# Kernel tuning notes

Measured on AMD Instinct MI355X. Metric: run time of the kernel, lower is better.

Reference implementation:

```python
import jax, jax.numpy as jnp
import numpy as np

B, C, V, K, H, W = 1, 3, 9, 8, 512, 512


def setup_inputs() -> dict:
    key = jax.random.key(0)
    k0, k1 = jax.random.split(key, 2)
    x = jax.random.normal(k0, (B, C, K, H, W), jnp.float32)          # FDL layers (spatial)
    y_views = jax.random.normal(k1, (B, C, V, H, W), jnp.float32)    # observed views (spatial)
    g = jnp.arange(3, dtype=jnp.float32) - 1.0                       # 3x3 camera grid positions
    uu, vv = jnp.meshgrid(g, g, indexing='ij')
    u = uu.reshape(-1)
    v = vv.reshape(-1)
    d = jnp.linspace(-2.0, 2.0, K).astype(jnp.float32)               # d_fdl disparities
    rho = jnp.full((1,), 0.3, jnp.float32)
    return {"x": x, "y_views": y_views, "u": u, "v": v, "d": d, "rho": rho}


def _pack_half_spectrum(Xf, x_c, y_c, n_proc):
    # [..., H, W] -> transpose to [..., W, H], center-roll so zero freq is at (x_c-1, y_c-1),
    # flatten x-major, keep the non-redundant half spectrum (first n_proc entries).
    Xt = jnp.swapaxes(Xf, -1, -2)
    Xt = jnp.roll(Xt, shift=(x_c - 1, y_c - 1), axis=(-2, -1))
    sh = Xt.shape
    return Xt.reshape(sh[:-2] + (sh[-2] * sh[-1],))[..., :n_proc]


def reference(x, y_views, u, v, d, rho):
    Bn, Cn, Kn = x.shape[0], x.shape[1], x.shape[2]
    Hn, Wn = x.shape[-2], x.shape[-1]
    rho = rho.reshape(())
    x_c = (Wn + 2) // 2                      # ceil((W+1)/2)
    y_c = (Hn + 2) // 2
    n_proc = Hn * (x_c - 1) + y_c            # half-spectrum size
    e0 = 1 - Hn % 2
    e1 = 1 - Wn % 2

    X = jnp.fft.fft2(x)                      # [B,C,K,H,W] complex64
    Y = jnp.fft.fft2(y_views)                # [B,C,V,H,W] complex64
    Xp = jnp.moveaxis(_pack_half_spectrum(X, x_c, y_c, n_proc), 2, 3) * rho   # [B,C,F,K]
    Yp = jnp.moveaxis(_pack_half_spectrum(Y, x_c, y_c, n_proc), 2, 3)         # [B,C,F,V]

    # centered angular frequency grids, flattened x-major to match packing order
    wx = (jnp.arange(Wn, dtype=jnp.float32) - (x_c - 1)) * (2.0 * np.pi / Wn)
    wy = (jnp.arange(Hn, dtype=jnp.float32) - (y_c - 1)) * (2.0 * np.pi / Hn)
    wx_f = jnp.repeat(wx, Hn)[:n_proc]       # [F]
    wy_f = jnp.tile(wy, Wn)[:n_proc]         # [F]

    # FDL data matrix A[f,v,k] = exp(i * d_k * (u_v*wx_f + v_v*wy_f))
    shift = u[None, :] * wx_f[:, None] + v[None, :] * wy_f[:, None]   # [F,V]
    A = jnp.exp(1j * shift[:, :, None] * d[None, None, :])            # [F,V,K] complex64
    Ah = jnp.conj(A)
    ATA = jnp.einsum('fvk,fvl->fkl', Ah, A)                           # [F,K,K]
    ATb = jnp.einsum('fvk,bcfv->bcfk', Ah, Yp)                        # [B,C,F,K]
    M = ATA + rho * jnp.eye(Kn, dtype=ATA.dtype)
    fdl = jnp.linalg.solve(M, (ATb + Xp)[..., None])[..., 0]          # [B,C,F,K]

    # pad redundant half with zeros, restore [B,C,K,H,W] layout
    fdl = jnp.pad(fdl, ((0, 0), (0, 0), (0, Hn * Wn - n_proc), (0, 0)))
    fdl = fdl.reshape(Bn, Cn, Wn, Hn, Kn).transpose(0, 1, 4, 3, 2)    # [B,C,K,H,W]

    # Hermitian (conjugate) symmetry reconstruction
    fdl = fdl.at[..., y_c:, x_c - 1:].set(jnp.conj(fdl[..., e0:y_c - 1, e1:x_c][..., ::-1, ::-1]))
    fdl = fdl.at[..., e0:y_c, x_c:].set(jnp.conj(fdl[..., y_c - 1:, e1:x_c - 1][..., ::-1, ::-1]))
    fdl = jnp.roll(fdl, shift=(1 - y_c, 1 - x_c), axis=(-2, -1))
    return jnp.fft.ifft2(fdl).real
```

## Files before the change

kernel.cpp:

```cpp
#include <hip/hip_runtime.h>
#include <math.h>

constexpr int N    = 512;
constexpr int LOGN = 9;
constexpr int NN   = N * N;
constexpr int CCH  = 3;
constexpr int KK   = 8;
constexpr int VV   = 9;
constexpr int FHALF = N * (N / 2) + (N / 2 + 1);
constexpr float PI_F = 3.14159265358979323846f;

__device__ __forceinline__ float2 cmulf(float2 a, float2 b) {
    return make_float2(a.x * b.x - a.y * b.y, a.x * b.y + a.y * b.x);
}
__device__ __forceinline__ float2 cadd(float2 a, float2 b) { return make_float2(a.x + b.x, a.y + b.y); }
__device__ __forceinline__ float2 csub(float2 a, float2 b) { return make_float2(a.x - b.x, a.y - b.y); }

template<int SG>
__device__ __forceinline__ float2 cmuli(float2 z) {
    return (SG < 0) ? make_float2(z.y, -z.x) : make_float2(-z.y, z.x);
}

template<int SG>
__device__ __forceinline__ void dft8(float2 x[8]) {
    const float c = 0.70710678118654752440f;
    float2 a0 = cadd(x[0], x[4]), a1 = cadd(x[1], x[5]);
    float2 a2 = cadd(x[2], x[6]), a3 = cadd(x[3], x[7]);
    float2 d0 = csub(x[0], x[4]), d1 = csub(x[1], x[5]);
    float2 d2 = csub(x[2], x[6]), d3 = csub(x[3], x[7]);
    float2 b0 = d0;
    float2 b1 = cmulf(d1, make_float2(c, (float)SG * c));
    float2 b2 = cmuli<SG>(d2);
    float2 b3 = cmulf(d3, make_float2(-c, (float)SG * c));
    float2 aa0 = cadd(a0, a2), aa1 = cadd(a1, a3);
    float2 ab0 = csub(a0, a2), ab1 = cmuli<SG>(csub(a1, a3));
    float2 ba0 = cadd(b0, b2), ba1 = cadd(b1, b3);
    float2 bb0 = csub(b0, b2), bb1 = cmuli<SG>(csub(b1, b3));
    x[0] = cadd(aa0, aa1); x[4] = csub(aa0, aa1);
    x[2] = cadd(ab0, ab1); x[6] = csub(ab0, ab1);
    x[1] = cadd(ba0, ba1); x[5] = csub(ba0, ba1);
    x[3] = cadd(bb0, bb1); x[7] = csub(bb0, bb1);
}

__device__ __forceinline__ void twiddle8(float2 v[8], float base) {
    float sn, cs;
    __sincosf(base, &sn, &cs);
    float2 w1 = make_float2(cs, sn);
    float2 wk = w1;
    v[1] = cmulf(v[1], wk);
    #pragma unroll
    for (int k = 2; k < 8; ++k) { wk = cmulf(wk, w1); v[k] = cmulf(v[k], wk); }
}

template<int SG>
__device__ __forceinline__ void wave_fft512(float2 v[8], float* sre, float* sim,
                                            int t, int stride, int off) {
    int t1 = t >> 3, t0 = t & 7;
    dft8<SG>(v);
    twiddle8(v, (float)SG * (2.0f * PI_F / 512.0f) * (float)t);
    #pragma unroll
    for (int k = 0; k < 8; ++k) {
        int a = (68 * k + 8 * t1 + t0) * stride + off;
        sre[a] = v[k].x; sim[a] = v[k].y;
    }
    #pragma unroll
    for (int n = 0; n < 8; ++n) {
        int a = (68 * t1 + 8 * n + t0) * stride + off;
        v[n] = make_float2(sre[a], sim[a]);
    }
    dft8<SG>(v);
    twiddle8(v, (float)SG * (2.0f * PI_F / 64.0f) * (float)t0);
    #pragma unroll
    for (int k = 0; k < 8; ++k) {
        int a = (68 * t0 + 8 * k + t1) * stride + off;
        sre[a] = v[k].x; sim[a] = v[k].y;
    }
    #pragma unroll
    for (int n = 0; n < 8; ++n) {
        int a = (68 * n + 8 * t0 + t1) * stride + off;
        v[n] = make_float2(sre[a], sim[a]);
    }
    dft8<SG>(v);
}

__global__ __launch_bounds__(256) void k_fft_r2c_rows_pack(const float* __restrict__ inx,
                                                           const float* __restrict__ iny,
                                                           int nximg,
                                                           float2* __restrict__ out) {
    __shared__ float sre[4][544];
    __shared__ float sim[4][544];
    int w = threadIdx.x >> 6, t = threadIdx.x & 63;
    long long gp = (long long)blockIdx.x * 4 + w;
    long long row0 = gp * 2;
    long long xrows = (long long)nximg * N;
    const float* src0 = (row0 < xrows) ? (inx + row0 * N)
                                       : (iny + (row0 - xrows) * N);
    const float* src1 = src0 + N;
    float2 v[8];
    #pragma unroll
    for (int e = 0; e < 8; ++e) v[e] = make_float2(src0[t + 64 * e], src1[t + 64 * e]);
    wave_fft512<-1>(v, sre[w], sim[w], t, 1, 0);
    int kb = (t >> 3) + 8 * (t & 7);
    #pragma unroll
    for (int k0 = 0; k0 < 8; ++k0) {
        int p = kb + 64 * k0;
        sre[w][p] = v[k0].x; sim[w][p] = v[k0].y;
    }
    float2* dst0 = out + row0 * N;
    float2* dst1 = dst0 + N;
    #pragma unroll
    for (int k0 = 4; k0 < 8; ++k0) {
        int p  = kb + 64 * k0;
        int mp = 512 - p;
        float zmx = sre[w][mp], zmy = sim[w][mp];
        float2 Zp = v[k0];
        dst0[p] = make_float2(0.5f * (Zp.x + zmx), 0.5f * (Zp.y - zmy));
        dst1[p] = make_float2(0.5f * (Zp.y + zmy), 0.5f * (zmx - Zp.x));
    }
    if (t == 0) {
        dst0[0] = make_float2(v[0].x, 0.0f);
        dst1[0] = make_float2(v[0].y, 0.0f);
    }
}

__global__ __launch_bounds__(256) void k_fft_r2c_rows(const float* __restrict__ in,
                                                      float2* __restrict__ out) {
    __shared__ float sre[4][544];
    __shared__ float sim[4][544];
    int w = threadIdx.x >> 6, t = threadIdx.x & 63;
    long long grow = (long long)blockIdx.x * 4 + w;
    const float* src = in + grow * N;
    float2 v[8];
    #pragma unroll
    for (int e = 0; e < 8; ++e) v[e] = make_float2(src[t + 64 * e], 0.0f);
    wave_fft512<-1>(v, sre[w], sim[w], t, 1, 0);
    float2* dst = out + grow * N;
    int kb = (t >> 3) + 8 * (t & 7);
    #pragma unroll
    for (int k0 = 0; k0 < 8; ++k0) dst[kb + 64 * k0] = v[k0];
}

template<int SG>
__global__ __launch_bounds__(256) void k_fft_pairswap(float2* __restrict__ data,
                                                      float scale, int lex, int sex) {
    __shared__ float sre[4][544];
    __shared__ float sim[4][544];
    int w = threadIdx.x >> 6, t = threadIdx.x & 63;
    int b = blockIdx.x;
    long long imgBase = (long long)(b >> 7) * NN;
    int pa = (b & 127) << 1;
    int rowg = pa + (w & 1) + ((w >> 1) << 8);
    const float2* src = data + imgBase + (long long)rowg * N;
    float2 v[8];
    #pragma unroll
    for (int e = 0; e < 8; ++e) v[e] = src[t + 64 * (e ^ lex)];
    __syncthreads();
    wave_fft512<SG>(v, sre[w], sim[w], t, 1, 0);
    float2* dst = data + imgBase + (long long)(rowg ^ 256) * N;
    int kb = (t >> 3) + 8 * (t & 7);
    #pragma unroll
    for (int k0 = 0; k0 < 8; ++k0) {
        float2 z = v[k0];
        dst[kb + 64 * (k0 ^ sex)] = make_float2(z.x * scale, z.y * scale);
    }
}

__global__ __launch_bounds__(256) void k_fft_cols_fwd(const float2* __restrict__ in,
                                                      float2* __restrict__ out) {
    __shared__ float tre[4896];
    __shared__ float tim[4896];
    int t = threadIdx.x;
    long long imgOff = (long long)blockIdx.y * NN;
    int bx = blockIdx.x;
    int x0 = bx ? (248 + (bx << 3)) : 0;
    {
        int xi2 = (t & 3) << 1;
        int yb  = t >> 2;
        const float2* img = in + imgOff;
        #pragma unroll
        for (int it = 0; it < 8; ++it) {
            int y = it * 64 + yb;
            float4 q = *(const float4*)&img[(long long)y * N + x0 + xi2];
            int a = y * 9 + xi2;
            tre[a] = q.x; tim[a] = q.y; tre[a + 1] = q.z; tim[a + 1] = q.w;
        }
    }
    __syncthreads();
    int w = t >> 6, lane = t & 63;
    int kb = (lane >> 3) + 8 * (lane & 7);
    #pragma unroll
    for (int r = 0; r < 2; ++r) {
        int cc = (w << 1) | r;
        float2 v[8];
        #pragma unroll
        for (int e = 0; e < 8; ++e) {
            int a = (lane + 64 * e) * 9 + cc;
            v[e] = make_float2(tre[a], tim[a]);
        }
        wave_fft512<-1>(v, tre, tim, lane, 9, cc);
        #pragma unroll
        for (int k0 = 0; k0 < 8; ++k0) {
            int a = (kb + 64 * k0) * 9 + cc;
            tre[a] = v[k0].x; tim[a] = v[k0].y;
        }
    }
    __syncthreads();
    {
        int xi = t >> 5, co = t & 31;
        float2* orow = out + imgOff + (long long)((x0 + xi) ^ 256) * N;
        #pragma unroll
        for (int it = 0; it < 8; ++it) {
            int b = it * 64 + co * 2;
            int y1 = b ^ 256;
            int a1 = y1 * 9 + xi, a2 = (y1 + 1) * 9 + xi;
            *(float4*)&orow[b] = make_float4(tre[a1], tim[a1], tre[a2], tim[a2]);
        }
    }
}

__device__ __forceinline__ void accum_pair(float2 bacc[KK], float tr[KK], float s,
                                           float d0, float dlt, float2 Yp, float2 Yn) {
    float2 Sp = make_float2(Yp.x + Yn.x, Yp.y + Yn.y);
    float2 Dm = make_float2(Yp.x - Yn.x, Yp.y - Yn.y);
    float sn, cs;
    __sincosf(s * d0, &sn, &cs);  float2 p = make_float2(cs, sn);
    __sincosf(s * dlt, &sn, &cs); float2 q = make_float2(cs, sn);
    float2 w = q;
    #pragma unroll
    for (int k = 0; k < KK; ++k) {
        bacc[k].x += p.x * Sp.x + p.y * Dm.y;
        bacc[k].y += p.x * Sp.y - p.y * Dm.x;
        if (k < KK - 1) {
            p = cmulf(p, q);
            tr[k + 1] += 2.0f * w.x;
            w = cmulf(w, q);
        }
    }
}

__device__ __forceinline__ void solve_point(float2 bacc[KK], float tr[KK], float rho) {
    float diag = tr[0] + rho;
    float L[36], Li[KK];
    #pragma unroll
    for (int j = 0; j < KK; ++j) {
        float acc = diag;
        #pragma unroll
        for (int t = 0; t < j; ++t) { float l = L[(j * (j - 1)) / 2 + t]; acc -= l * l; }
        float dj = sqrtf(acc);
        float inv = 1.0f / dj;
        Li[j] = inv;
        #pragma unroll
        for (int i = j + 1; i < KK; ++i) {
            float a = tr[i - j];
            #pragma unroll
            for (int t = 0; t < j; ++t)
                a -= L[(i * (i - 1)) / 2 + t] * L[(j * (j - 1)) / 2 + t];
            L[(i * (i - 1)) / 2 + j] = a * inv;
        }
    }
    #pragma unroll
    for (int i = 0; i < KK; ++i) {
        float2 a = bacc[i];
        #pragma unroll
        for (int t = 0; t < i; ++t) {
            float l = L[(i * (i - 1)) / 2 + t];
            a.x -= l * bacc[t].x;
            a.y -= l * bacc[t].y;
        }
        bacc[i] = make_float2(a.x * Li[i], a.y * Li[i]);
    }
    #pragma unroll
    for (int i = KK - 1; i >= 0; --i) {
        float2 a = bacc[i];
        #pragma unroll
        for (int t = i + 1; t < KK; ++t) {
            float l = L[(t * (t - 1)) / 2 + i];
            a.x -= l * bacc[t].x;
            a.y -= l * bacc[t].y;
        }
        bacc[i] = make_float2(a.x * Li[i], a.y * Li[i]);
    }
}

__global__ __launch_bounds__(256) void k_solve_ifft(const float2* __restrict__ Xs,
                                                    const float2* __restrict__ Ys,
                                                    float2* __restrict__ P,
                                                    const float* __restrict__ uu,
                                                    const float* __restrict__ vv,
                                                    const float* __restrict__ dd,
                                                    const float* __restrict__ rhop) {
    __shared__ float gre[KK][N];
    __shared__ float gim[KK][N];
    __shared__ float fsre[4][544];
    __shared__ float fsim[4][544];
    int a  = blockIdx.x;
    int ch = blockIdx.y;
    int t  = threadIdx.x;
    float rho = rhop[0];
    float d0 = dd[0], dlt = dd[1] - dd[0];
    const float C = 2.0f * PI_F / (float)N;
    float wxv = (float)(a - 256) * C;
    const float2* Xrow = Xs + (long long)ch * KK * NN + (long long)a * N;
    const float2* Yrow = Ys + (long long)ch * VV * NN + (long long)a * N;
    float wy0 = (float)(t - 256) * C;
    float wy1 = (float)(t)       * C;

    float2 bacc0[KK], bacc1[KK];
    float tr0[KK], tr1[KK];
    {
        const float2* Yc = Yrow + (long long)4 * NN;
        float2 yc0 = Yc[t], yc1 = Yc[t + 256];
        #pragma unroll
        for (int k = 0; k < KK; ++k) { bacc0[k] = yc0; bacc1[k] = yc1; }
        tr0[0] = tr1[0] = (float)VV;
        #pragma unroll
        for (int l = 1; l < KK; ++l) { tr0[l] = 1.0f; tr1[l] = 1.0f; }
    }
    #pragma unroll
    for (int j = 0; j < 4; ++j) {
        int vp = 5 + j, vn = 3 - j;
        float su = uu[vp], sv = vv[vp];
        const float2* Ypr = Yrow + (long long)vp * NN;
        const float2* Ynr = Yrow + (long long)vn * NN;
        float2 Yp0 = Ypr[t], Yn0 = Ynr[t];
        float2 Yp1 = Ypr[t + 256], Yn1 = Ynr[t + 256];
        accum_pair(bacc0, tr0, su * wxv + sv * wy0, d0, dlt, Yp0, Yn0);
        accum_pair(bacc1, tr1, su * wxv + sv * wy1, d0, dlt, Yp1, Yn1);
    }
    #pragma unroll
    for (int k = 0; k < KK; ++k) {
        const float2* Xr = Xrow + (long long)k * NN;
        float2 x0v = Xr[t], x1v = Xr[t + 256];
        bacc0[k].x += rho * x0v.x; bacc0[k].y += rho * x0v.y;
        bacc1[k].x += rho * x1v.x; bacc1[k].y += rho * x1v.y;
    }
    solve_point(bacc0, tr0, rho);
    solve_point(bacc1, tr1, rho);
    #pragma unroll
    for (int k = 0; k < KK; ++k) {
        gre[k][t] = bacc0[k].x;       gim[k][t] = bacc0[k].y;
        gre[k][t + 256] = bacc1[k].x; gim[k][t + 256] = bacc1[k].y;
    }
    __syncthreads();
    if (a == 256 && t >= 1) {
        int b = t + 256, bs = 256 - t;
        #pragma unroll
        for (int k = 0; k < KK; ++k) {
            gre[k][b] = gre[k][bs];
            gim[k][b] = -gim[k][bs];
        }
    }
    __syncthreads();

    int w = t >> 6, lane = t & 63;
    int kb = (lane >> 3) + 8 * (lane & 7);
    float sgn = ((lane >> 3) & 1) ? -1.0f : 1.0f;
    const float inv512 = 1.0f / 512.0f;
    #pragma unroll
    for (int r = 0; r < 2; ++r) {
        int k = (w << 1) | r;
        float2 v[8];
        #pragma unroll
        for (int e = 0; e < 8; ++e) {
            int idx = (lane + 64 * e) ^ 256;
            v[e] = make_float2(gre[k][idx], gim[k][idx]);
        }
        wave_fft512<1>(v, fsre[w], fsim[w], lane, 1, 0);
        float s0x = gre[k][0], s0y = gim[k][0];
        float2* Pimg = P + (long long)(ch * KK + k) * NN;
        if (a >= 1 && a <= 255) {
            float2* pmain = Pimg + (long long)(a + 256) * N;
            float2* pmirr = Pimg + (long long)(256 - a) * N;
            #pragma unroll
            for (int k0 = 0; k0 < 8; ++k0) {
                int pos = kb + 64 * k0;
                float2 W = v[k0];
                pmain[pos] = make_float2(W.x * inv512, W.y * inv512);
                pmirr[pos] = make_float2((W.x - s0x * sgn) * inv512,
                                         (-W.y + s0y * sgn) * inv512);
            }
        } else {
            float2* pmain = Pimg + (long long)(a == 0 ? 256 : 0) * N;
            #pragma unroll
            for (int k0 = 0; k0 < 8; ++k0) {
                int pos = kb + 64 * k0;
                float2 W = v[k0];
                pmain[pos] = make_float2(W.x * inv512, W.y * inv512);
            }
        }
    }
}

__global__ __launch_bounds__(256) void k_fft_cols_inv_real(const float2* __restrict__ in,
                                                           float* __restrict__ out,
                                                           float scale) {
    __shared__ float tre[4896];
    __shared__ float tim[4896];
    int t = threadIdx.x;
    long long imgOff = (long long)blockIdx.y * NN;
    int b0 = blockIdx.x << 3;
    {
        int xi2 = (t & 3) << 1;
        int yb  = t >> 2;
        const float2* img = in + imgOff;
        #pragma unroll
        for (int it = 0; it < 8; ++it) {
            int c = it * 64 + yb;
            float4 q = *(const float4*)&img[(long long)c * N + b0 + xi2];
            int a = c * 9 + xi2;
            tre[a] = q.x; tim[a] = q.y; tre[a + 1] = q.z; tim[a + 1] = q.w;
        }
    }
    __syncthreads();
    int w = t >> 6, lane = t & 63;
    int kb = (lane >> 3) + 8 * (lane & 7);
    #pragma unroll
    for (int r = 0; r < 2; ++r) {
        int cc = (w << 1) | r;
        float2 v[8];
        #pragma unroll
        for (int e = 0; e < 8; ++e) {
            int a = (lane + 64 * e) * 9 + cc;
            v[e] = make_float2(tre[a], tim[a]);
        }
        wave_fft512<1>(v, tre, tim, lane, 9, cc);
        #pragma unroll
        for (int k0 = 0; k0 < 8; ++k0)
            tre[(kb + 64 * k0) * 9 + cc] = v[k0].x;
    }
    __syncthreads();
    {
        int xi = t >> 5, co = t & 31;
        float* orow = out + (long long)blockIdx.y * NN + (long long)(b0 + xi) * N;
        #pragma unroll
        for (int it = 0; it < 4; ++it) {
            int ww = it * 128 + co * 4;
            *(float4*)&orow[ww] = make_float4(tre[ww * 9 + xi] * scale,
                                              tre[(ww + 1) * 9 + xi] * scale,
                                              tre[(ww + 2) * 9 + xi] * scale,
                                              tre[(ww + 3) * 9 + xi] * scale);
        }
    }
}

__global__ __launch_bounds__(256) void k_transpose_inplace(float2* __restrict__ data) {
    int ti = blockIdx.x, tj = blockIdx.y;
    if (ti > tj) return;
    float2* img = data + (long long)blockIdx.z * NN;
    __shared__ float2 ta[32][33];
    __shared__ float2 tb[32][33];
    int tx = threadIdx.x, ty = threadIdx.y;
    int r0 = ti << 5, c0 = tj << 5;
    bool diag = (ti == tj);
    #pragma unroll
    for (int kk = 0; kk < 4; ++kk) {
        int r = ty + (kk << 3);
        ta[r][tx] = img[(long long)(r0 + r) * N + (c0 + tx)];
        if (!diag) tb[r][tx] = img[(long long)(c0 + r) * N + (r0 + tx)];
    }
    __syncthreads();
    #pragma unroll
    for (int kk = 0; kk < 4; ++kk) {
        int r = ty + (kk << 3);
        img[(long long)(c0 + r) * N + (r0 + tx)] = ta[tx][r];
        if (!diag) img[(long long)(r0 + r) * N + (c0 + tx)] = tb[tx][r];
    }
}

__global__ __launch_bounds__(256) void k_fft_c2r_rows(const float2* __restrict__ in,
                                                      float* __restrict__ out, float scale) {
    __shared__ float sre[4][544];
    __shared__ float sim[4][544];
    int w = threadIdx.x >> 6, t = threadIdx.x & 63;
    long long grow = (long long)blockIdx.x * 4 + w;
    const float2* src = in + grow * N;
    float2 v[8];
    #pragma unroll
    for (int e = 0; e < 8; ++e) v[e] = src[t + 64 * e];
    wave_fft512<1>(v, sre[w], sim[w], t, 1, 0);
    float* dst = out + grow * N;
    int kb = (t >> 3) + 8 * (t & 7);
    #pragma unroll
    for (int k0 = 0; k0 < 8; ++k0) dst[kb + 64 * k0] = v[k0].x * scale;
}

__global__ __launch_bounds__(256) void k_solve(float2* __restrict__ Xs,
                                               const float2* __restrict__ Ys,
                                               const float* __restrict__ uu,
                                               const float* __restrict__ vv,
                                               const float* __restrict__ dd,
                                               const float* __restrict__ rhop) {
    int f = blockIdx.x * 256 + threadIdx.x;
    if (f >= FHALF) return;
    long long coffX = (long long)blockIdx.y * KK * NN;
    long long coffY = (long long)blockIdx.y * VV * NN;
    float rho = rhop[0];
    int x = f >> LOGN;
    int y = f & (N - 1);
    float wxv = (float)(x - N / 2) * (2.0f * PI_F / (float)N);
    float wyv = (float)(y - N / 2) * (2.0f * PI_F / (float)N);
    float d0 = dd[0], dlt = dd[1] - dd[0];
    float2 bacc[KK];
    float tr[KK];
    {
        float2 Yc = Ys[coffY + (long long)4 * NN + f];
        #pragma unroll
        for (int k = 0; k < KK; ++k) bacc[k] = Yc;
        tr[0] = (float)VV;
        #pragma unroll
        for (int l = 1; l < KK; ++l) tr[l] = 1.0f;
    }
    #pragma unroll
    for (int j = 0; j < 4; ++j) {
        int vp = 5 + j, vn = 3 - j;
        float s = uu[vp] * wxv + vv[vp] * wyv;
        accum_pair(bacc, tr, s, d0, dlt,
                   Ys[coffY + (long long)vp * NN + f],
                   Ys[coffY + (long long)vn * NN + f]);
    }
    #pragma unroll
    for (int k = 0; k < KK; ++k) {
        float2 Xk = Xs[coffX + (long long)k * NN + f];
        bacc[k].x += rho * Xk.x;
        bacc[k].y += rho * Xk.y;
    }
    solve_point(bacc, tr, rho);
    int xm = (N - x) & (N - 1);
    int ym = (N - y) & (N - 1);
    long long fm = (long long)xm * N + ym;
    bool conjMirror = false, zeroMirror = false;
    if (x >= 1 && x <= N / 2 - 1) {
        if (y == 0) zeroMirror = true; else conjMirror = true;
    } else if (x == N / 2 && y >= 1 && y <= N / 2 - 1) {
        conjMirror = true;
    }
    #pragma unroll
    for (int k = 0; k < KK; ++k) {
        float2* base = Xs + coffX + (long long)k * NN;
        float2 z = bacc[k];
        base[f] = z;
        if (conjMirror)      base[fm] = make_float2(z.x, -z.y);
        else if (zeroMirror) base[fm] = make_float2(0.f, 0.f);
    }
}

extern "C" void kernel_launch(void* const* d_in, const int* in_sizes, int n_in,
                              void* d_out, int out_size, void* d_ws, size_t ws_size,
                              hipStream_t stream) {
    (void)in_sizes; (void)n_in; (void)out_size;
    const float* x   = (const float*)d_in[0];
    const float* yv  = (const float*)d_in[1];
    const float* uu  = (const float*)d_in[2];
    const float* vvp = (const float*)d_in[3];
    const float* dd  = (const float*)d_in[4];
    const float* rho = (const float*)d_in[5];
    float* out = (float*)d_out;
    float2* ws = (float2*)d_ws;

    const size_t needBatchedPack = (size_t)2 * CCH * (KK + VV) * NN * sizeof(float2);
    const size_t needChanPack    = (size_t)2 * (KK + VV) * NN * sizeof(float2);
    const float invN = 1.0f / (float)N;

    if (ws_size >= needChanPack) {
        bool batched = ws_size >= needBatchedPack;
        int iters = batched ? 1 : CCH;
        int ncs   = batched ? CCH : 1;
        int nx = ncs * KK, ny = ncs * VV;
        for (int it = 0; it < iters; ++it) {
            float2* Xt = ws;
            float2* Yt = ws + (size_t)nx * NN;
            float2* Rt = ws + (size_t)(nx + ny) * NN;
            const float* xin = x  + (size_t)it * KK * NN;
            const float* yin = yv + (size_t)it * VV * NN;
            float* oout = out + (size_t)it * KK * NN;
            k_fft_r2c_rows_pack<<<(nx + ny) * (N / 8), 256, 0, stream>>>(xin, yin, nx, Rt);
            k_fft_cols_fwd<<<dim3(33, nx + ny), 256, 0, stream>>>(Rt, Xt);
            k_solve_ifft<<<dim3(257, ncs), 256, 0, stream>>>(Xt, Yt, Rt, uu, vvp, dd, rho);
            k_fft_cols_inv_real<<<dim3(N / 8, nx), 256, 0, stream>>>(Rt, oout, invN);
        }
    } else {
        for (int it = 0; it < CCH; ++it) {
            float2* Xb = ws;
            float2* Yb = ws + (size_t)KK * NN;
            const float* xin = x  + (size_t)it * KK * NN;
            const float* yin = yv + (size_t)it * VV * NN;
            float* oout = out + (size_t)it * KK * NN;
            k_fft_r2c_rows<<<KK * (N / 4), 256, 0, stream>>>(xin, Xb);
            k_fft_r2c_rows<<<VV * (N / 4), 256, 0, stream>>>(yin, Yb);
            k_transpose_inplace<<<dim3(16, 16, KK), dim3(32, 8), 0, stream>>>(Xb);
            k_transpose_inplace<<<dim3(16, 16, VV), dim3(32, 8), 0, stream>>>(Yb);
            k_fft_pairswap<-1><<<KK * (N / 4), 256, 0, stream>>>(Xb, 1.0f, 0, 4);
            k_fft_pairswap<-1><<<VV * (N / 4), 256, 0, stream>>>(Yb, 1.0f, 0, 4);
            k_solve<<<dim3((FHALF + 255) / 256, 1), 256, 0, stream>>>(Xb, Yb, uu, vvp, dd, rho);
            k_fft_pairswap<1><<<KK * (N / 4), 256, 0, stream>>>(Xb, invN, 4, 0);
            k_transpose_inplace<<<dim3(16, 16, KK), dim3(32, 8), 0, stream>>>(Xb);
            k_fft_c2r_rows<<<KK * (N / 4), 256, 0, stream>>>(Xb, oout, invN);
        }
    }
}
```

Before: 179.5 us.

## Reconstruct mirrored spectrum rows in inverse column FFT instead of storing them

The solve+row-IFFT kernel no longer writes the Hermitian-mirrored half of the intermediate spectrum. It stores only a small per-row DC correction term (S0), and the inverse column FFT kernel rebuilds the mirrored rows in shared memory from the main rows plus that term. This roughly halves global writes and reads of the intermediate buffer at the cost of extra index arithmetic and a small side buffer. The forward column kernel also skips redundant FFT columns and row stores in block 0.

New measurement: 172.9 us. 3.7% less time.

```diff
diff --git a/kernel.cpp b/kernel.cpp
--- a/kernel.cpp
+++ b/kernel.cpp
@@ -191,6 +191,7 @@
     #pragma unroll
     for (int r = 0; r < 2; ++r) {
         int cc = (w << 1) | r;
+        if (bx == 0 && cc != 0) continue;
         float2 v[8];
         #pragma unroll
         for (int e = 0; e < 8; ++e) {
@@ -207,13 +208,15 @@
     __syncthreads();
     {
         int xi = t >> 5, co = t & 31;
-        float2* orow = out + imgOff + (long long)((x0 + xi) ^ 256) * N;
-        #pragma unroll
-        for (int it = 0; it < 8; ++it) {
-            int b = it * 64 + co * 2;
-            int y1 = b ^ 256;
-            int a1 = y1 * 9 + xi, a2 = (y1 + 1) * 9 + xi;
-            *(float4*)&orow[b] = make_float4(tre[a1], tim[a1], tre[a2], tim[a2]);
+        if (!(bx == 0 && xi != 0)) {
+            float2* orow = out + imgOff + (long long)((x0 + xi) ^ 256) * N;
+            #pragma unroll
+            for (int it = 0; it < 8; ++it) {
+                int b = it * 64 + co * 2;
+                int y1 = b ^ 256;
+                int a1 = y1 * 9 + xi, a2 = (y1 + 1) * 9 + xi;
+                *(float4*)&orow[b] = make_float4(tre[a1], tim[a1], tre[a2], tim[a2]);
+            }
         }
     }
 }
@@ -285,6 +288,7 @@
 __global__ __launch_bounds__(256) void k_solve_ifft(const float2* __restrict__ Xs,
                                                     const float2* __restrict__ Ys,
                                                     float2* __restrict__ P,
+                                                    float2* __restrict__ S0,
                                                     const float* __restrict__ uu,
                                                     const float* __restrict__ vv,
                                                     const float* __restrict__ dd,
@@ -354,7 +358,6 @@
 
     int w = t >> 6, lane = t & 63;
     int kb = (lane >> 3) + 8 * (lane & 7);
-    float sgn = ((lane >> 3) & 1) ? -1.0f : 1.0f;
     const float inv512 = 1.0f / 512.0f;
     #pragma unroll
     for (int r = 0; r < 2; ++r) {
@@ -367,31 +370,23 @@
         }
         wave_fft512<1>(v, fsre[w], fsim[w], lane, 1, 0);
         float s0x = gre[k][0], s0y = gim[k][0];
+        if (lane == 0)
+            S0[(long long)(ch * KK + k) * 257 + a] =
+                make_float2(s0x * inv512, s0y * inv512);
         float2* Pimg = P + (long long)(ch * KK + k) * NN;
-        if (a >= 1 && a <= 255) {
-            float2* pmain = Pimg + (long long)(a + 256) * N;
-            float2* pmirr = Pimg + (long long)(256 - a) * N;
-            #pragma unroll
-            for (int k0 = 0; k0 < 8; ++k0) {
-                int pos = kb + 64 * k0;
-                float2 W = v[k0];
-                pmain[pos] = make_float2(W.x * inv512, W.y * inv512);
-                pmirr[pos] = make_float2((W.x - s0x * sgn) * inv512,
-                                         (-W.y + s0y * sgn) * inv512);
-            }
-        } else {
-            float2* pmain = Pimg + (long long)(a == 0 ? 256 : 0) * N;
-            #pragma unroll
-            for (int k0 = 0; k0 < 8; ++k0) {
-                int pos = kb + 64 * k0;
-                float2 W = v[k0];
-                pmain[pos] = make_float2(W.x * inv512, W.y * inv512);
-            }
+        int prow = (a >= 1 && a <= 255) ? (a + 256) : (a == 0 ? 256 : 0);
+        float2* pmain = Pimg + (long long)prow * N;
+        #pragma unroll
+        for (int k0 = 0; k0 < 8; ++k0) {
+            int pos = kb + 64 * k0;
+            float2 W = v[k0];
+            pmain[pos] = make_float2(W.x * inv512, W.y * inv512);
         }
     }
 }
 
 __global__ __launch_bounds__(256) void k_fft_cols_inv_real(const float2* __restrict__ in,
+                                                           const float2* __restrict__ T0,
                                                            float* __restrict__ out,
                                                            float scale) {
     __shared__ float tre[4896];
@@ -403,12 +398,29 @@
         int xi2 = (t & 3) << 1;
         int yb  = t >> 2;
         const float2* img = in + imgOff;
-        #pragma unroll
-        for (int it = 0; it < 8; ++it) {
-            int c = it * 64 + yb;
-            float4 q = *(const float4*)&img[(long long)c * N + b0 + xi2];
-            int a = c * 9 + xi2;
-            tre[a] = q.x; tim[a] = q.y; tre[a + 1] = q.z; tim[a + 1] = q.w;
+        const float2* T0i = T0 + (long long)blockIdx.y * 257;
+        #pragma unroll
+        for (int it = 0; it < 4; ++it) {
+            int p = 256 + it * 64 + yb;
+            float4 q = *(const float4*)&img[(long long)p * N + b0 + xi2];
+            int c = p * 9 + xi2;
+            tre[c] = q.x; tim[c] = q.y; tre[c + 1] = q.z; tim[c + 1] = q.w;
+            if (p > 256) {
+                float2 t0 = T0i[p - 256];
+                int m0 = b0 + xi2;
+                float sg0 = (m0 & 1) ? -1.0f : 1.0f;
+                float sg1 = -sg0;
+                int cm = (512 - p) * 9 + xi2;
+                tre[cm]     = q.x - t0.x * sg0;
+                tim[cm]     = -q.y + t0.y * sg0;
+                tre[cm + 1] = q.z - t0.x * sg1;
+                tim[cm + 1] = -q.w + t0.y * sg1;
+            }
+        }
+        if (t < 4) {
+            int xi2b = t << 1;
+            float4 q = *(const float4*)&img[(long long)(b0 + xi2b)];
+            tre[xi2b] = q.x; tim[xi2b] = q.y; tre[xi2b + 1] = q.z; tim[xi2b + 1] = q.w;
         }
     }
     __syncthreads();
@@ -557,8 +569,11 @@
     float* out = (float*)d_out;
     float2* ws = (float2*)d_ws;
 
-    const size_t needBatchedPack = (size_t)2 * CCH * (KK + VV) * NN * sizeof(float2);
-    const size_t needChanPack    = (size_t)2 * (KK + VV) * NN * sizeof(float2);
+    const size_t s0Elems = (size_t)CCH * KK * 257;
+    const size_t needBatchedPack =
+        (size_t)2 * CCH * (KK + VV) * NN * sizeof(float2) + s0Elems * sizeof(float2);
+    const size_t needChanPack =
+        (size_t)2 * (KK + VV) * NN * sizeof(float2) + (size_t)KK * 257 * sizeof(float2);
     const float invN = 1.0f / (float)N;
 
     if (ws_size >= needChanPack) {
@@ -570,13 +585,14 @@
             float2* Xt = ws;
             float2* Yt = ws + (size_t)nx * NN;
             float2* Rt = ws + (size_t)(nx + ny) * NN;
+            float2* S0 = ws + (size_t)2 * (nx + ny) * NN;
             const float* xin = x  + (size_t)it * KK * NN;
             const float* yin = yv + (size_t)it * VV * NN;
             float* oout = out + (size_t)it * KK * NN;
             k_fft_r2c_rows_pack<<<(nx + ny) * (N / 8), 256, 0, stream>>>(xin, yin, nx, Rt);
             k_fft_cols_fwd<<<dim3(33, nx + ny), 256, 0, stream>>>(Rt, Xt);
-            k_solve_ifft<<<dim3(257, ncs), 256, 0, stream>>>(Xt, Yt, Rt, uu, vvp, dd, rho);
-            k_fft_cols_inv_real<<<dim3(N / 8, nx), 256, 0, stream>>>(Rt, oout, invN);
+            k_solve_ifft<<<dim3(257, ncs), 256, 0, stream>>>(Xt, Yt, Rt, S0, uu, vvp, dd, rho);
+            k_fft_cols_inv_real<<<dim3(N / 8, nx), 256, 0, stream>>>(Rt, S0, oout, invN);
         }
     } else {
         for (int it = 0; it < CCH; ++it) {
```
